# Kernel tuning notes

Hardware: AMD Instinct MI355X
Metric: run time of the kernel (lower is better)

The kernel has to match this reference:

```python
import jax, jax.numpy as jnp
import numpy as np

B, T, E, H = 512, 256, 384, 64

def setup_inputs() -> dict:
    key = jax.random.key(0)
    k1, k2, k3, k4 = jax.random.split(key, 4)
    scale = 1.0 / np.sqrt(E)
    return {
        "x":  jax.random.normal(k1, (B, T, E), dtype=jnp.float32),
        "Wq": jax.random.normal(k2, (E, H), dtype=jnp.float32) * scale,
        "Wk": jax.random.normal(k3, (E, H), dtype=jnp.float32) * scale,
        "Wv": jax.random.normal(k4, (E, H), dtype=jnp.float32) * scale,
    }

def reference(x, Wq, Wk, Wv):
    # single-head causal self-attention (dropout in eval mode / identity)
    q = jnp.einsum('bte,eh->bth', x, Wq)
    k = jnp.einsum('bte,eh->bth', x, Wk)
    v = jnp.einsum('bte,eh->bth', x, Wv)
    d = q.shape[-1]
    wei = jnp.einsum('bqh,bkh->bqk', q, k) * (d ** -0.5)   # [B,T,T]
    T_ = x.shape[1]
    causal = jnp.tril(jnp.ones((T_, T_), dtype=bool))
    wei = jnp.where(causal[None, :, :], wei, -jnp.inf)
    wei = jax.nn.softmax(wei, axis=-1)
    out = jnp.einsum('bqk,bkh->bqh', wei, v)               # [B,T,H]
    return out
```

## Files before the change

### kernel.cpp

```cpp
#include <hip/hip_runtime.h>

typedef __attribute__((ext_vector_type(4)))  float f32x4;
typedef __attribute__((ext_vector_type(16))) float f32x16;
typedef __attribute__((ext_vector_type(8)))  short s16x8;
typedef __attribute__((ext_vector_type(4)))  short s16x4;


__device__ inline short f2bf(float f){
  unsigned u = __float_as_uint(f);
  u = u + 0x7fffu + ((u >> 16) & 1u);
  return (short)(u >> 16);
}

__global__ void wt_prep_kernel(const float* __restrict__ Wq, const float* __restrict__ Wk,
                               const float* __restrict__ Wv, short* __restrict__ Wt){
  int o = blockIdx.x * 256 + threadIdx.x;
  if (o >= 192*384) return;
  int n = o / 384, k = o - n*384;
  const float* W = (n < 64) ? Wq : (n < 128) ? Wk : Wv;
  Wt[o] = f2bf(W[k*64 + (n & 63)]);
}

__global__ __launch_bounds__(512, 2) void fused_kernel(const float* __restrict__ x,
                             const short* __restrict__ Wt, float* __restrict__ out){
  __shared__ __align__(16) short Qs[256*72];
  __shared__ __align__(16) short Ks[256*72];
  __shared__ __align__(16) short Vts[64*264];
  __shared__ __align__(16) short Pp[8][16*40];

  const int tid  = threadIdx.x;
  const int w    = tid >> 6, lane = tid & 63;
  const int l31  = lane & 31, hh = lane >> 5;
  const int b    = blockIdx.x;

  const float* xb = x + ((long)b*256 + w*32)*384;

  f32x16 acc[6];
  #pragma unroll
  for (int c = 0; c < 6; ++c)
    #pragma unroll
    for (int j = 0; j < 16; ++j) acc[c][j] = 0.0f;

  #pragma unroll 2
  for (int kt = 0; kt < 6; ++kt){
    #pragma unroll
    for (int s = 0; s < 4; ++s){
      const int k0 = kt*64 + s*16 + hh*8;
      const float* xp = xb + l31*384 + k0;
      float4 a0 = *(const float4*)xp;
      float4 a1 = *(const float4*)(xp + 4);
      s16x8 bx;
      bx[0]=f2bf(a0.x); bx[1]=f2bf(a0.y); bx[2]=f2bf(a0.z); bx[3]=f2bf(a0.w);
      bx[4]=f2bf(a1.x); bx[5]=f2bf(a1.y); bx[6]=f2bf(a1.z); bx[7]=f2bf(a1.w);
      #pragma unroll
      for (int c = 0; c < 6; ++c){
        s16x8 wa = *(const s16x8*)(Wt + (c*32 + l31)*384 + k0);
        acc[c] = __builtin_amdgcn_mfma_f32_32x32x16_bf16(wa, bx, acc[c], 0, 0, 0);
      }
    }
  }

  const int trow = w*32 + l31;
  #pragma unroll
  for (int c = 0; c < 4; ++c){
    short* dst = (c < 2) ? Qs : Ks;
    const int nb = (c & 1)*32;
    #pragma unroll
    for (int g = 0; g < 4; ++g){
      s16x4 v;
      #pragma unroll
      for (int i = 0; i < 4; ++i) v[i] = f2bf(acc[c][g*4 + i]);
      *(s16x4*)(dst + trow*72 + nb + 8*g + 4*hh) = v;
    }
  }
  #pragma unroll
  for (int c = 4; c < 6; ++c)
    #pragma unroll
    for (int reg = 0; reg < 16; ++reg){
      const int h = (c-4)*32 + (reg & 3) + 8*(reg >> 2) + 4*hh;
      Vts[h*264 + trow] = f2bf(acc[c][reg]);
    }

  __syncthreads();

  const int l15 = lane & 15, quad = lane >> 4;
  float* ob = out + (long)b*256*64;
  short* Pw = Pp[w];

  for (int it = 0; it < 2; ++it){
    const int F  = it ? (15 - w) : w;
    const int qb = F*16;
    const int NF = F + 1;
    const int NS = (NF + 1) >> 1;

    s16x8 qf0 = *(const s16x8*)(Qs + (qb + l15)*72 + quad*8);
    s16x8 qf1 = *(const s16x8*)(Qs + (qb + l15)*72 + 32 + quad*8);

    f32x4 sc[16];
    #pragma unroll
    for (int f = 0; f < 16; ++f){
      f32x4 a;
      #pragma unroll
      for (int r = 0; r < 4; ++r) a[r] = 0.0f;
      if (f < NF){
        const short* kp = Ks + (f*16 + l15)*72 + quad*8;
        s16x8 k0v = *(const s16x8*)kp;
        s16x8 k1v = *(const s16x8*)(kp + 32);
        a = __builtin_amdgcn_mfma_f32_16x16x32_bf16(qf0, k0v, a, 0, 0, 0);
        a = __builtin_amdgcn_mfma_f32_16x16x32_bf16(qf1, k1v, a, 0, 0, 0);
      }
      sc[f] = a;
    }

    float mx[4], sm[4];
    #pragma unroll
    for (int r = 0; r < 4; ++r) mx[r] = -3.0e38f;
    #pragma unroll
    for (int f = 0; f < 16; ++f){
      if (f < NF){
        const int key = f*16 + l15;
        #pragma unroll
        for (int r = 0; r < 4; ++r){
          const int qg = qb + quad*4 + r;
          float s = sc[f][r] * 0.125f;
          s = (key <= qg) ? s : -1.0e30f;
          sc[f][r] = s;
          mx[r] = fmaxf(mx[r], s);
        }
      }
    }
    #pragma unroll
    for (int r = 0; r < 4; ++r){
      #pragma unroll
      for (int off = 1; off < 16; off <<= 1) mx[r] = fmaxf(mx[r], __shfl_xor(mx[r], off, 16));
    }
    #pragma unroll
    for (int r = 0; r < 4; ++r) sm[r] = 0.0f;
    #pragma unroll
    for (int f = 0; f < 16; ++f){
      if (f < NF){
        #pragma unroll
        for (int r = 0; r < 4; ++r){
          float p = exp2f((sc[f][r] - mx[r]) * 1.44269504f);
          sc[f][r] = p;
          sm[r] += p;
        }
      }
    }
    #pragma unroll
    for (int r = 0; r < 4; ++r){
      #pragma unroll
      for (int off = 1; off < 16; off <<= 1) sm[r] += __shfl_xor(sm[r], off, 16);
    }

    f32x4 o[4];
    #pragma unroll
    for (int h0 = 0; h0 < 4; ++h0)
      #pragma unroll
      for (int r = 0; r < 4; ++r) o[h0][r] = 0.0f;

    #pragma unroll
    for (int ks = 0; ks < 8; ++ks){
      if (ks < NS){
        #pragma unroll
        for (int fi = 0; fi < 2; ++fi){
          const int f = 2*ks + fi;
          #pragma unroll
          for (int r = 0; r < 4; ++r){
            short v = 0;
            if (f < NF) v = f2bf(sc[f][r]);
            Pw[(quad*4 + r)*40 + fi*16 + l15] = v;
          }
        }
        s16x8 pf = *(const s16x8*)(Pw + l15*40 + quad*8);
        #pragma unroll
        for (int h0 = 0; h0 < 4; ++h0){
          s16x8 vf = *(const s16x8*)(Vts + (h0*16 + l15)*264 + ks*32 + quad*8);
          o[h0] = __builtin_amdgcn_mfma_f32_16x16x32_bf16(pf, vf, o[h0], 0, 0, 0);
        }
      }
    }

    #pragma unroll
    for (int r = 0; r < 4; ++r){
      const float inv = 1.0f / sm[r];
      #pragma unroll
      for (int h0 = 0; h0 < 4; ++h0)
        ob[(qb + quad*4 + r)*64 + h0*16 + l15] = o[h0][r] * inv;
    }
  }
}

extern "C" void kernel_launch(void* const* d_in, const int* in_sizes, int n_in,
                              void* d_out, int out_size, void* d_ws, size_t ws_size,
                              hipStream_t stream){
  const float* x  = (const float*)d_in[0];
  const float* Wq = (const float*)d_in[1];
  const float* Wk = (const float*)d_in[2];
  const float* Wv = (const float*)d_in[3];
  float* out = (float*)d_out;

  short* Wt = (short*)d_ws;

  hipLaunchKernelGGL(wt_prep_kernel, dim3(288), dim3(256), 0, stream, Wq, Wk, Wv, Wt);
  hipLaunchKernelGGL(fused_kernel,   dim3(512), dim3(512), 0, stream, x, Wt, out);
}
```

Baseline: 361.8 us.

## Move V to global workspace and split projection columns to raise occupancy

V is now written to a global workspace instead of shared memory. Q fragments are preloaded into registers so the Q buffer can be reused as the P staging area. Together these cut LDS use per block, and the launch bounds now ask for four blocks per CU. The projection is re-split so each wave computes 96 output columns for two row groups, with a register prefetch of the next x slice, which lowers accumulator pressure. In exchange, V loads during the PV matmul come from global/L2 rather than LDS, and each x row is read twice. The tighter register cap may also cause spills.

```diff
diff --git a/kernel.cpp b/kernel.cpp
--- a/kernel.cpp
+++ b/kernel.cpp
@@ -21,80 +21,93 @@
   Wt[o] = f2bf(W[k*64 + (n & 63)]);
 }
 
-__global__ __launch_bounds__(512, 2) void fused_kernel(const float* __restrict__ x,
-                             const short* __restrict__ Wt, float* __restrict__ out){
+__global__ __launch_bounds__(512, 4) void fused_kernel(const float* __restrict__ x,
+                             const short* __restrict__ Wt, short* __restrict__ Vg,
+                             float* __restrict__ out){
   __shared__ __align__(16) short Qs[256*72];
   __shared__ __align__(16) short Ks[256*72];
-  __shared__ __align__(16) short Vts[64*264];
-  __shared__ __align__(16) short Pp[8][16*40];
 
   const int tid  = threadIdx.x;
   const int w    = tid >> 6, lane = tid & 63;
   const int l31  = lane & 31, hh = lane >> 5;
   const int b    = blockIdx.x;
-
-  const float* xb = x + ((long)b*256 + w*32)*384;
-
-  f32x16 acc[6];
-  #pragma unroll
-  for (int c = 0; c < 6; ++c)
-    #pragma unroll
-    for (int j = 0; j < 16; ++j) acc[c][j] = 0.0f;
-
-  #pragma unroll 2
-  for (int kt = 0; kt < 6; ++kt){
-    #pragma unroll
-    for (int s = 0; s < 4; ++s){
-      const int k0 = kt*64 + s*16 + hh*8;
-      const float* xp = xb + l31*384 + k0;
-      float4 a0 = *(const float4*)xp;
-      float4 a1 = *(const float4*)(xp + 4);
+  const int ch   = (w & 1) * 96;
+  short* Vb = Vg + (long)b*64*256;
+
+  for (int j = 0; j < 2; ++j){
+    const int rg   = (w >> 1) + j*4;
+    const int trow = rg*32 + l31;
+    const float* xp = x + ((long)b*256 + trow)*384 + hh*8;
+
+    f32x16 acc[3];
+    #pragma unroll
+    for (int c = 0; c < 3; ++c)
+      #pragma unroll
+      for (int q = 0; q < 16; ++q) acc[c][q] = 0.0f;
+
+    float4 c0 = *(const float4*)xp;
+    float4 c1 = *(const float4*)(xp + 4);
+    #pragma unroll
+    for (int s = 0; s < 24; ++s){
+      float4 n0, n1;
+      if (s < 23){
+        n0 = *(const float4*)(xp + (s+1)*16);
+        n1 = *(const float4*)(xp + (s+1)*16 + 4);
+      }
       s16x8 bx;
-      bx[0]=f2bf(a0.x); bx[1]=f2bf(a0.y); bx[2]=f2bf(a0.z); bx[3]=f2bf(a0.w);
-      bx[4]=f2bf(a1.x); bx[5]=f2bf(a1.y); bx[6]=f2bf(a1.z); bx[7]=f2bf(a1.w);
-      #pragma unroll
-      for (int c = 0; c < 6; ++c){
-        s16x8 wa = *(const s16x8*)(Wt + (c*32 + l31)*384 + k0);
+      bx[0]=f2bf(c0.x); bx[1]=f2bf(c0.y); bx[2]=f2bf(c0.z); bx[3]=f2bf(c0.w);
+      bx[4]=f2bf(c1.x); bx[5]=f2bf(c1.y); bx[6]=f2bf(c1.z); bx[7]=f2bf(c1.w);
+      #pragma unroll
+      for (int c = 0; c < 3; ++c){
+        s16x8 wa = *(const s16x8*)(Wt + (ch + c*32 + l31)*384 + s*16 + hh*8);
         acc[c] = __builtin_amdgcn_mfma_f32_32x32x16_bf16(wa, bx, acc[c], 0, 0, 0);
       }
+      c0 = n0; c1 = n1;
+    }
+
+    #pragma unroll
+    for (int c = 0; c < 3; ++c){
+      const int n0 = ch + c*32;
+      if (n0 < 128){
+        short* dst = (n0 < 64) ? (Qs + trow*72 + n0) : (Ks + trow*72 + (n0 - 64));
+        #pragma unroll
+        for (int g = 0; g < 4; ++g){
+          s16x4 v;
+          #pragma unroll
+          for (int i = 0; i < 4; ++i) v[i] = f2bf(acc[c][g*4 + i]);
+          *(s16x4*)(dst + 8*g + 4*hh) = v;
+        }
+      } else {
+        #pragma unroll
+        for (int reg = 0; reg < 16; ++reg){
+          const int h = (n0 - 128) + (reg & 3) + 8*(reg >> 2) + 4*hh;
+          Vb[h*256 + trow] = f2bf(acc[c][reg]);
+        }
+      }
     }
   }
-
-  const int trow = w*32 + l31;
-  #pragma unroll
-  for (int c = 0; c < 4; ++c){
-    short* dst = (c < 2) ? Qs : Ks;
-    const int nb = (c & 1)*32;
-    #pragma unroll
-    for (int g = 0; g < 4; ++g){
-      s16x4 v;
-      #pragma unroll
-      for (int i = 0; i < 4; ++i) v[i] = f2bf(acc[c][g*4 + i]);
-      *(s16x4*)(dst + trow*72 + nb + 8*g + 4*hh) = v;
-    }
-  }
-  #pragma unroll
-  for (int c = 4; c < 6; ++c)
-    #pragma unroll
-    for (int reg = 0; reg < 16; ++reg){
-      const int h = (c-4)*32 + (reg & 3) + 8*(reg >> 2) + 4*hh;
-      Vts[h*264 + trow] = f2bf(acc[c][reg]);
-    }
-
   __syncthreads();
 
   const int l15 = lane & 15, quad = lane >> 4;
   float* ob = out + (long)b*256*64;
-  short* Pw = Pp[w];
-
+
+  const int Fs[2] = { w, 15 - w };
+  s16x8 qa[2][2];
+  #pragma unroll
   for (int it = 0; it < 2; ++it){
-    const int F  = it ? (15 - w) : w;
+    qa[it][0] = *(const s16x8*)(Qs + (Fs[it]*16 + l15)*72 + quad*8);
+    qa[it][1] = *(const s16x8*)(Qs + (Fs[it]*16 + l15)*72 + 32 + quad*8);
+  }
+  __syncthreads();
+  short* Pw = Qs + w*1280;
+
+  #pragma unroll
+  for (int it = 0; it < 2; ++it){
+    const int F  = Fs[it];
     const int qb = F*16;
     const int NF = F + 1;
     const int NS = (NF + 1) >> 1;
-
-    s16x8 qf0 = *(const s16x8*)(Qs + (qb + l15)*72 + quad*8);
-    s16x8 qf1 = *(const s16x8*)(Qs + (qb + l15)*72 + 32 + quad*8);
+    const s16x8 qf0 = qa[it][0], qf1 = qa[it][1];
 
     f32x4 sc[16];
     #pragma unroll
@@ -175,7 +188,7 @@
         s16x8 pf = *(const s16x8*)(Pw + l15*40 + quad*8);
         #pragma unroll
         for (int h0 = 0; h0 < 4; ++h0){
-          s16x8 vf = *(const s16x8*)(Vts + (h0*16 + l15)*264 + ks*32 + quad*8);
+          s16x8 vf = *(const s16x8*)(Vb + (h0*16 + l15)*256 + ks*32 + quad*8);
           o[h0] = __builtin_amdgcn_mfma_f32_16x16x32_bf16(pf, vf, o[h0], 0, 0, 0);
         }
       }
@@ -200,8 +213,10 @@
   const float* Wv = (const float*)d_in[3];
   float* out = (float*)d_out;
 
-  short* Wt = (short*)d_ws;
+  char* ws = (char*)d_ws;
+  short* Wt = (short*)ws;
+  short* Vg = (short*)(ws + 147456);
 
   hipLaunchKernelGGL(wt_prep_kernel, dim3(288), dim3(256), 0, stream, Wq, Wk, Wv, Wt);
-  hipLaunchKernelGGL(fused_kernel,   dim3(512), dim3(512), 0, stream, x, Wt, out);
-}
+  hipLaunchKernelGGL(fused_kernel,   dim3(512), dim3(512), 0, stream, x, Wt, Vg, out);
+}
```

Result: slower. 498.9 us (+37.9%).
